# Optimization experiments

Measured on AMD Instinct MI355X. Metric: run time of the kernel, lower is better.

The kernel has to match this reference:

```python
import jax, jax.numpy as jnp
import numpy as np

HEADS = 16
DIM_HEAD = 64
QUERY_DIM = 1024
INNER = HEADS * DIM_HEAD
SCALE = DIM_HEAD ** -0.5


def setup_inputs() -> dict:
    key = jax.random.key(0)
    ks = jax.random.split(key, 6)
    B, N, M = 2, 2048, 2048
    x = jax.random.normal(ks[0], (B, N, QUERY_DIM), dtype=jnp.float32)
    context = jax.random.normal(ks[1], (B, M, QUERY_DIM), dtype=jnp.float32)
    s = QUERY_DIM ** -0.5
    # weights stored [in, out] so y = x @ W matches torch Linear(x) with W = weight.T
    Wq = jax.random.normal(ks[2], (QUERY_DIM, INNER), dtype=jnp.float32) * s
    Wk = jax.random.normal(ks[3], (QUERY_DIM, INNER), dtype=jnp.float32) * s
    Wv = jax.random.normal(ks[4], (QUERY_DIM, INNER), dtype=jnp.float32) * s
    Wo = jax.random.normal(ks[5], (INNER, QUERY_DIM), dtype=jnp.float32) * (INNER ** -0.5)
    return {"x": x, "context": context, "Wq": Wq, "Wk": Wk, "Wv": Wv, "Wo": Wo}


def reference(x, context, Wq, Wk, Wv, Wo):
    B, N, _ = x.shape
    M = context.shape[1]
    # projections -> [b, n, h, d]
    q = (x @ Wq).reshape(B, N, HEADS, DIM_HEAD)
    k = (context @ Wk).reshape(B, M, HEADS, DIM_HEAD)
    v = (context @ Wv).reshape(B, M, HEADS, DIM_HEAD)
    sim = jnp.einsum('bihd,bjhd->bhij', q, k) * SCALE  # [b, h, n, m]
    attn = jax.nn.softmax(sim, axis=-1)
    out = jnp.einsum('bhij,bjhd->bihd', attn, v)  # [b, n, h, d]
    out = out.reshape(B, N, INNER)
    return out @ Wo
```

## Files before the change

kernel.cpp:

```cpp
#include <hip/hip_runtime.h>
#include <hip/hip_bf16.h>


typedef __attribute__((ext_vector_type(8))) __bf16    bf16x8;
typedef __attribute__((ext_vector_type(4))) __bf16    bf16x4;
typedef __attribute__((ext_vector_type(4))) float     f32x4;

#define B_    2
#define H_    16
#define N_    2048
#define M_    2048
#define D_    64
#define QD_   1024

#define QSCALE 0.18033688011112042f

__device__ __forceinline__ void gld16(const __bf16* g, __bf16* l) {
    __builtin_amdgcn_global_load_lds(
        (const __attribute__((address_space(1))) unsigned int*)(g),
        (__attribute__((address_space(3))) unsigned int*)(l), 16, 0, 0);
}

__global__ __launch_bounds__(256) void prep(const float* __restrict__ x,
                                            const float* __restrict__ ctx,
                                            const float* __restrict__ w0,
                                            const float* __restrict__ w1,
                                            const float* __restrict__ w2,
                                            const float* __restrict__ w3,
                                            __bf16* __restrict__ xb,
                                            __bf16* __restrict__ cb,
                                            __bf16* __restrict__ t0,
                                            __bf16* __restrict__ t1,
                                            __bf16* __restrict__ t2,
                                            __bf16* __restrict__ t3) {
    __shared__ float tile[64][65];
    const int z = blockIdx.z;
    if (z < 2) {
        const float* src = z ? ctx : x;
        __bf16*      dst = z ? cb  : xb;
        const size_t base = (size_t)(blockIdx.y * 16 + blockIdx.x) * 16384;
#pragma unroll
        for (int p = 0; p < 16; ++p) {
            size_t i = base + p * 1024 + threadIdx.x * 4;
            float4 v = *reinterpret_cast<const float4*>(src + i);
            bf16x4 o;
            o.x = (__bf16)v.x; o.y = (__bf16)v.y; o.z = (__bf16)v.z; o.w = (__bf16)v.w;
            *reinterpret_cast<bf16x4*>(dst + i) = o;
        }
        return;
    }
    const int w = z - 2;
    const float* in = (w == 0) ? w0 : (w == 1) ? w1 : (w == 2) ? w2 : w3;
    __bf16*     out = (w == 0) ? t0 : (w == 1) ? t1 : (w == 2) ? t2 : t3;
    const int i0 = blockIdx.x * 64;
    const int o0 = blockIdx.y * 64;
    const int t  = threadIdx.x;
    const int r  = t >> 4;
    const int c4 = (t & 15) * 4;
#pragma unroll
    for (int p = 0; p < 4; ++p) {
        int row = p * 16 + r;
        float4 v = *reinterpret_cast<const float4*>(in + (size_t)(i0 + row) * QD_ + o0 + c4);
        tile[row][c4 + 0] = v.x; tile[row][c4 + 1] = v.y;
        tile[row][c4 + 2] = v.z; tile[row][c4 + 3] = v.w;
    }
    __syncthreads();
#pragma unroll
    for (int p = 0; p < 4; ++p) {
        int orow = p * 16 + r;
        bf16x4 o;
        o.x = (__bf16)tile[c4 + 0][orow];
        o.y = (__bf16)tile[c4 + 1][orow];
        o.z = (__bf16)tile[c4 + 2][orow];
        o.w = (__bf16)tile[c4 + 3][orow];
        *reinterpret_cast<bf16x4*>(out + (size_t)(o0 + orow) * QD_ + i0 + c4) = o;
    }
}

__global__ __launch_bounds__(256) void gemm_qkv(const __bf16* __restrict__ xb,
                                                const __bf16* __restrict__ cb,
                                                const __bf16* __restrict__ Wtq,
                                                const __bf16* __restrict__ Wtk,
                                                const __bf16* __restrict__ Wtv,
                                                __bf16* __restrict__ Qb,
                                                __bf16* __restrict__ Kb,
                                                __bf16* __restrict__ Vt) {
    __shared__ __align__(16) __bf16 POOL[16384];
    __bf16* const Al0 = POOL;
    __bf16* const Al1 = POOL + 4096;
    __bf16* const Bl0 = POOL + 8192;
    __bf16* const Bl1 = POOL + 12288;

    const int z = blockIdx.z;
    const __bf16* A_  = (z == 0) ? xb : cb;
    const __bf16* Bt_ = (z == 0) ? Wtq : (z == 1) ? Wtk : Wtv;

    const int tid  = threadIdx.x;
    const int wid  = tid >> 6;
    const int lane = tid & 63;
    const int l15  = lane & 15;
    const int lg   = lane >> 4;
    const int wr   = wid >> 1;
    const int wc   = wid & 1;
    const int rowBase = blockIdx.x * 128;
    const int colBase = blockIdx.y * 128;
    const int srow = wid * 32 + (lane >> 2);
    const int sg   = ((lane & 3) ^ ((srow >> 1) & 3)) * 8;
    const __bf16* Ag  = A_  + (size_t)(rowBase + srow) * QD_ + sg;
    const __bf16* Ag2 = Ag  + (size_t)16 * QD_;
    const __bf16* Bg  = Bt_ + (size_t)(colBase + srow) * QD_ + sg;
    const __bf16* Bg2 = Bg  + (size_t)16 * QD_;
    const int sOff  = (wid * 32) * 32;
    const int sOff2 = sOff + 16 * 32;
    int aoff[4], boff[4];
#pragma unroll
    for (int m = 0; m < 4; ++m) {
        int ra = wr * 64 + m * 16 + l15;
        int rb = wc * 64 + m * 16 + l15;
        aoff[m] = ra * 32 + ((lg ^ ((ra >> 1) & 3)) * 8);
        boff[m] = rb * 32 + ((lg ^ ((rb >> 1) & 3)) * 8);
    }
    f32x4 acc[4][4] = {};

#define GCOMPUTE(AL, BL)                                                                       \
    {                                                                                          \
        bf16x8 a[4], b[4];                                                                     \
        _Pragma("unroll")                                                                      \
        for (int m = 0; m < 4; ++m)                                                            \
            a[m] = *reinterpret_cast<const bf16x8*>(&(AL)[aoff[m]]);                           \
        _Pragma("unroll")                                                                      \
        for (int n = 0; n < 4; ++n)                                                            \
            b[n] = *reinterpret_cast<const bf16x8*>(&(BL)[boff[n]]);                           \
        _Pragma("unroll")                                                                      \
        for (int m = 0; m < 4; ++m)                                                            \
            _Pragma("unroll")                                                                  \
            for (int n = 0; n < 4; ++n)                                                        \
                acc[m][n] = __builtin_amdgcn_mfma_f32_16x16x32_bf16(a[m], b[n], acc[m][n], 0, 0, 0); \
    }

    gld16(Ag,  Al0 + sOff);
    gld16(Ag2, Al0 + sOff2);
    gld16(Bg,  Bl0 + sOff);
    gld16(Bg2, Bl0 + sOff2);
    __syncthreads();
    for (int t = 0; t < 32; t += 2) {
        if (t + 1 < 32) {
            int kn = (t + 1) * 32;
            gld16(Ag + kn,  Al1 + sOff);
            gld16(Ag2 + kn, Al1 + sOff2);
            gld16(Bg + kn,  Bl1 + sOff);
            gld16(Bg2 + kn, Bl1 + sOff2);
        }
        GCOMPUTE(Al0, Bl0)
        __syncthreads();
        if (t + 2 < 32) {
            int kn = (t + 2) * 32;
            gld16(Ag + kn,  Al0 + sOff);
            gld16(Ag2 + kn, Al0 + sOff2);
            gld16(Bg + kn,  Bl0 + sOff);
            gld16(Bg2 + kn, Bl0 + sOff2);
        }
        GCOMPUTE(Al1, Bl1)
        __syncthreads();
    }
#undef GCOMPUTE

#pragma unroll
    for (int m = 0; m < 4; ++m)
#pragma unroll
        for (int n = 0; n < 4; ++n)
#pragma unroll
            for (int r = 0; r < 4; ++r) {
                float v = acc[m][n][r];
                if (z == 0) v *= QSCALE;
                int rl = wr * 64 + m * 16 + lg * 4 + r;
                int cl = wc * 64 + n * 16 + l15;
                if (z == 2) POOL[cl * 128 + rl] = (__bf16)v;
                else        POOL[rl * 128 + cl] = (__bf16)v;
            }
    __syncthreads();

    const int prow0 = tid >> 4;
    const int pcol  = (tid & 15) * 8;
#pragma unroll
    for (int s = 0; s < 8; ++s) {
        int row = s * 16 + prow0;
        bf16x8 vv = *reinterpret_cast<const bf16x8*>(&POOL[row * 128 + pcol]);
        if (z == 2) {
            int cc = colBase + row, rr = rowBase + pcol;
            int b_ = rr >> 11, mm = rr & 2047, hh = cc >> 6, dd = cc & 63;
            *reinterpret_cast<bf16x8*>(&Vt[((size_t)(b_ * H_ + hh) * D_ + dd) * M_ + mm]) = vv;
        } else {
            int rr = rowBase + row, cc = colBase + pcol;
            int b_ = rr >> 11, nn = rr & 2047, hh = cc >> 6, dd = cc & 63;
            __bf16* dst = (z == 0) ? Qb : Kb;
            *reinterpret_cast<bf16x8*>(&dst[((size_t)(b_ * H_ + hh) * N_ + nn) * D_ + dd]) = vv;
        }
    }
}

__global__ __launch_bounds__(256) void gemm_out(const __bf16* __restrict__ AO,
                                                const __bf16* __restrict__ Wto,
                                                float* __restrict__ out) {
    __shared__ __align__(16) __bf16 POOL[16384];
    __bf16* const Al0 = POOL;
    __bf16* const Al1 = POOL + 4096;
    __bf16* const Bl0 = POOL + 8192;
    __bf16* const Bl1 = POOL + 10240;

    const int tid  = threadIdx.x;
    const int wid  = tid >> 6;
    const int lane = tid & 63;
    const int l15  = lane & 15;
    const int lg   = lane >> 4;
    const int wr   = wid >> 1;
    const int wc   = wid & 1;
    const int rowBase = blockIdx.x * 128;
    const int colBase = blockIdx.y * 64;
    const int srowA = wid * 32 + (lane >> 2);
    const int srowB = wid * 16 + (lane >> 2);
    const int sgA   = ((lane & 3) ^ ((srowA >> 1) & 3)) * 8;
    const int sgB   = ((lane & 3) ^ ((srowB >> 1) & 3)) * 8;
    const __bf16* Ag  = AO  + (size_t)(rowBase + srowA) * QD_ + sgA;
    const __bf16* Ag2 = Ag  + (size_t)16 * QD_;
    const __bf16* Bg  = Wto + (size_t)(colBase + srowB) * QD_ + sgB;
    const int sOffA  = (wid * 32) * 32;
    const int sOffA2 = sOffA + 16 * 32;
    const int sOffB  = (wid * 16) * 32;
    int aoff[4], boff[2];
#pragma unroll
    for (int m = 0; m < 4; ++m) {
        int ra = wr * 64 + m * 16 + l15;
        aoff[m] = ra * 32 + ((lg ^ ((ra >> 1) & 3)) * 8);
    }
#pragma unroll
    for (int n = 0; n < 2; ++n) {
        int rb = wc * 32 + n * 16 + l15;
        boff[n] = rb * 32 + ((lg ^ ((rb >> 1) & 3)) * 8);
    }
    f32x4 acc[4][2] = {};

#define GCOMPUTE2(AL, BL)                                                                      \
    {                                                                                          \
        bf16x8 a[4], b[2];                                                                     \
        _Pragma("unroll")                                                                      \
        for (int m = 0; m < 4; ++m)                                                            \
            a[m] = *reinterpret_cast<const bf16x8*>(&(AL)[aoff[m]]);                           \
        _Pragma("unroll")                                                                      \
        for (int n = 0; n < 2; ++n)                                                            \
            b[n] = *reinterpret_cast<const bf16x8*>(&(BL)[boff[n]]);                           \
        _Pragma("unroll")                                                                      \
        for (int m = 0; m < 4; ++m)                                                            \
            _Pragma("unroll")                                                                  \
            for (int n = 0; n < 2; ++n)                                                        \
                acc[m][n] = __builtin_amdgcn_mfma_f32_16x16x32_bf16(a[m], b[n], acc[m][n], 0, 0, 0); \
    }

    gld16(Ag,  Al0 + sOffA);
    gld16(Ag2, Al0 + sOffA2);
    gld16(Bg,  Bl0 + sOffB);
    __syncthreads();
    for (int t = 0; t < 32; t += 2) {
        if (t + 1 < 32) {
            int kn = (t + 1) * 32;
            gld16(Ag + kn,  Al1 + sOffA);
            gld16(Ag2 + kn, Al1 + sOffA2);
            gld16(Bg + kn,  Bl1 + sOffB);
        }
        GCOMPUTE2(Al0, Bl0)
        __syncthreads();
        if (t + 2 < 32) {
            int kn = (t + 2) * 32;
            gld16(Ag + kn,  Al0 + sOffA);
            gld16(Ag2 + kn, Al0 + sOffA2);
            gld16(Bg + kn,  Bl0 + sOffB);
        }
        GCOMPUTE2(Al1, Bl1)
        __syncthreads();
    }
#undef GCOMPUTE2

    float* FP = reinterpret_cast<float*>(POOL);
#pragma unroll
    for (int m = 0; m < 4; ++m)
#pragma unroll
        for (int n = 0; n < 2; ++n)
#pragma unroll
            for (int r = 0; r < 4; ++r) {
                int rl = wr * 64 + m * 16 + lg * 4 + r;
                int cl = wc * 32 + n * 16 + l15;
                FP[rl * 64 + cl] = acc[m][n][r];
            }
    __syncthreads();
    const int prow0 = tid >> 4;
    const int pcol4 = (tid & 15) * 4;
#pragma unroll
    for (int s = 0; s < 8; ++s) {
        int row = s * 16 + prow0;
        float4 vv = *reinterpret_cast<const float4*>(&FP[row * 64 + pcol4]);
        *reinterpret_cast<float4*>(&out[(size_t)(rowBase + row) * QD_ + colBase + pcol4]) = vv;
    }
}

__global__ __launch_bounds__(512, 4) void attn_kernel(const __bf16* __restrict__ Q,
                                                      const __bf16* __restrict__ K,
                                                      const __bf16* __restrict__ Vt,
                                                      __bf16* __restrict__ AO) {
    __shared__ __align__(16) __bf16 Klds[2][4096];
    __shared__ __align__(16) __bf16 Vlds[2][4096];

    const int logical = (blockIdx.x & 7) * 64 + (blockIdx.x >> 3);
    const int qt   = logical & 15;
    const int bh   = logical >> 4;
    const int b    = bh >> 4;
    const int h    = bh & 15;
    const int wid  = threadIdx.x >> 6;
    const int lane = threadIdx.x & 63;
    const int l15  = lane & 15;
    const int lg   = lane >> 4;
    const int qbase = qt * 128 + wid * 16;

    const __bf16* Qp = Q  + ((size_t)bh * N_ + qbase) * D_;
    const __bf16* Kp = K  + (size_t)bh * M_ * D_;
    const __bf16* Vp = Vt + (size_t)bh * D_ * M_;

    const int rg   = lane >> 3;
    const int ch   = lane & 7;
    const int skw  = (rg & 3) | ((wid & 1) << 2);
    const int kc   = (ch ^ skw) << 3;
    const int vc   = (ch ^ rg) << 3;
    const int srow = wid * 8 + rg;
    const int ldst = wid * 512;

#define STAGE(BUF, KV0)                                                        \
    gld16(Kp + (size_t)((KV0) + srow) * D_ + kc, &Klds[BUF][ldst]);            \
    gld16(Vp + (size_t)srow * M_ + (KV0) + vc,  &Vlds[BUF][ldst]);

    const int rm0 = ((l15 >> 2) * 8) + (l15 & 3);
    const int sq  = (l15 & 7) << 3;
    const int ak00 = rm0 * 64 + (( 0 + lg * 8) ^ sq);
    const int ak01 = rm0 * 64 + ((32 + lg * 8) ^ sq);
    const int ak10 = ak00 + 256;
    const int ak11 = ak01 + 256;
    const int av0 = l15 * 64 + (( 0 + lg * 8) ^ sq);
    const int av1 = l15 * 64 + ((32 + lg * 8) ^ sq);

    bf16x8 qf0 = *reinterpret_cast<const bf16x8*>(Qp + (size_t)l15 * D_ +      lg * 8);
    bf16x8 qf1 = *reinterpret_cast<const bf16x8*>(Qp + (size_t)l15 * D_ + 32 + lg * 8);

    bf16x8 onesf;
#pragma unroll
    for (int j = 0; j < 8; ++j) onesf[j] = (__bf16)1.0f;

    f32x4 o0 = {}, o1 = {}, o2 = {}, o3 = {}, ors = {};

#define COMPUTE(KB, VB, KOFF, AV)                                                               \
    {                                                                                           \
        bf16x8 k00 = *reinterpret_cast<const bf16x8*>((KB) + ak00 + (KOFF));                    \
        bf16x8 k01 = *reinterpret_cast<const bf16x8*>((KB) + ak01 + (KOFF));                    \
        bf16x8 k10 = *reinterpret_cast<const bf16x8*>((KB) + ak10 + (KOFF));                    \
        bf16x8 k11 = *reinterpret_cast<const bf16x8*>((KB) + ak11 + (KOFF));                    \
        bf16x8 v0  = *reinterpret_cast<const bf16x8*>((VB) + (AV));                             \
        bf16x8 v1  = *reinterpret_cast<const bf16x8*>((VB) + (AV) + 1024);                      \
        bf16x8 v2  = *reinterpret_cast<const bf16x8*>((VB) + (AV) + 2048);                      \
        bf16x8 v3  = *reinterpret_cast<const bf16x8*>((VB) + (AV) + 3072);                      \
        f32x4 s0 = {}, s1 = {};                                                                 \
        s0 = __builtin_amdgcn_mfma_f32_16x16x32_bf16(k00, qf0, s0, 0, 0, 0);                    \
        s0 = __builtin_amdgcn_mfma_f32_16x16x32_bf16(k01, qf1, s0, 0, 0, 0);                    \
        s1 = __builtin_amdgcn_mfma_f32_16x16x32_bf16(k10, qf0, s1, 0, 0, 0);                    \
        s1 = __builtin_amdgcn_mfma_f32_16x16x32_bf16(k11, qf1, s1, 0, 0, 0);                    \
        bf16x8 pf;                                                                              \
        pf[0] = (__bf16)__builtin_amdgcn_exp2f(s0[0]);                                          \
        pf[1] = (__bf16)__builtin_amdgcn_exp2f(s0[1]);                                          \
        pf[2] = (__bf16)__builtin_amdgcn_exp2f(s0[2]);                                          \
        pf[3] = (__bf16)__builtin_amdgcn_exp2f(s0[3]);                                          \
        pf[4] = (__bf16)__builtin_amdgcn_exp2f(s1[0]);                                          \
        pf[5] = (__bf16)__builtin_amdgcn_exp2f(s1[1]);                                          \
        pf[6] = (__bf16)__builtin_amdgcn_exp2f(s1[2]);                                          \
        pf[7] = (__bf16)__builtin_amdgcn_exp2f(s1[3]);                                          \
        ors = __builtin_amdgcn_mfma_f32_16x16x32_bf16(pf, onesf, ors, 0, 0, 0);                 \
        o0 = __builtin_amdgcn_mfma_f32_16x16x32_bf16(pf, v0, o0, 0, 0, 0);                      \
        o1 = __builtin_amdgcn_mfma_f32_16x16x32_bf16(pf, v1, o1, 0, 0, 0);                      \
        o2 = __builtin_amdgcn_mfma_f32_16x16x32_bf16(pf, v2, o2, 0, 0, 0);                      \
        o3 = __builtin_amdgcn_mfma_f32_16x16x32_bf16(pf, v3, o3, 0, 0, 0);                      \
    }

    STAGE(0, 0)
    __syncthreads();

    for (int t = 0; t < 32; t += 2) {
        if (t + 1 < 32) { STAGE(1, (t + 1) * 64) }
        COMPUTE(Klds[0], Vlds[0], 0,    av0)
        COMPUTE(Klds[0], Vlds[0], 2048, av1)
        __syncthreads();
        if (t + 2 < 32) { STAGE(0, (t + 2) * 64) }
        COMPUTE(Klds[1], Vlds[1], 0,    av0)
        COMPUTE(Klds[1], Vlds[1], 2048, av1)
        __syncthreads();
    }
#undef STAGE
#undef COMPUTE

#pragma unroll
    for (int r = 0; r < 4; ++r) {
        float inv = 1.0f / ors[r];
        size_t row = ((size_t)b * N_ + qbase + lg * 4 + r) * QD_ + h * D_ + l15;
        AO[row +  0] = (__bf16)(o0[r] * inv);
        AO[row + 16] = (__bf16)(o1[r] * inv);
        AO[row + 32] = (__bf16)(o2[r] * inv);
        AO[row + 48] = (__bf16)(o3[r] * inv);
    }
}

extern "C" void kernel_launch(void* const* d_in, const int* in_sizes, int n_in,
                              void* d_out, int out_size, void* d_ws, size_t ws_size,
                              hipStream_t stream) {
    const float* x   = (const float*)d_in[0];
    const float* ctx = (const float*)d_in[1];
    const float* Wq  = (const float*)d_in[2];
    const float* Wk  = (const float*)d_in[3];
    const float* Wv  = (const float*)d_in[4];
    const float* Wo  = (const float*)d_in[5];

    char* ws = (char*)d_ws;
    __bf16* xb  = (__bf16*)(ws);
    __bf16* cb  = (__bf16*)(ws + (8u  << 20));
    __bf16* Wtq = (__bf16*)(ws + (16u << 20));
    __bf16* Wtk = (__bf16*)(ws + (18u << 20));
    __bf16* Wtv = (__bf16*)(ws + (20u << 20));
    __bf16* Wto = (__bf16*)(ws + (22u << 20));
    __bf16* Qb  = (__bf16*)(ws + (24u << 20));
    __bf16* Kb  = (__bf16*)(ws + (32u << 20));
    __bf16* Vt  = (__bf16*)(ws + (40u << 20));
    __bf16* AO  = (__bf16*)(ws + (48u << 20));

    prep<<<dim3(16, 16, 6), 256, 0, stream>>>(x, ctx, Wq, Wk, Wv, Wo,
                                              xb, cb, Wtq, Wtk, Wtv, Wto);
    gemm_qkv<<<dim3(32, 8, 3), 256, 0, stream>>>(xb, cb, Wtq, Wtk, Wtv, Qb, Kb, Vt);
    attn_kernel<<<512, 512, 0, stream>>>(Qb, Kb, Vt, AO);
    gemm_out<<<dim3(32, 16), 256, 0, stream>>>(AO, Wto, (float*)d_out);
}
```

Baseline: 109.1 us.

## Process 32 query rows per wave in attention to reuse K/V fragments

The attention kernel now runs 4 waves of 256 threads per block instead of 8, and each wave handles 32 query rows instead of 16. Each K and V fragment read from LDS therefore feeds two sets of MFMAs, halving LDS reads per unit of compute. Each thread now issues four global-to-LDS loads per stage instead of two, so the same 64-row tile is still staged per block, and the swizzle indices are rewritten to match. The cost is roughly double the accumulator and score registers per wave and fewer waves per block, which may lower occupancy and latency hiding.

```diff
diff --git a/kernel.cpp b/kernel.cpp
--- a/kernel.cpp
+++ b/kernel.cpp
@@ -302,10 +302,10 @@
     }
 }
 
-__global__ __launch_bounds__(512, 4) void attn_kernel(const __bf16* __restrict__ Q,
-                                                      const __bf16* __restrict__ K,
-                                                      const __bf16* __restrict__ Vt,
-                                                      __bf16* __restrict__ AO) {
+__global__ __launch_bounds__(256) void attn_kernel(const __bf16* __restrict__ Q,
+                                                   const __bf16* __restrict__ K,
+                                                   const __bf16* __restrict__ Vt,
+                                                   __bf16* __restrict__ AO) {
     __shared__ __align__(16) __bf16 Klds[2][4096];
     __shared__ __align__(16) __bf16 Vlds[2][4096];
 
@@ -318,41 +318,53 @@
     const int lane = threadIdx.x & 63;
     const int l15  = lane & 15;
     const int lg   = lane >> 4;
-    const int qbase = qt * 128 + wid * 16;
+    const int qbase = qt * 128 + wid * 32;
 
     const __bf16* Qp = Q  + ((size_t)bh * N_ + qbase) * D_;
     const __bf16* Kp = K  + (size_t)bh * M_ * D_;
     const __bf16* Vp = Vt + (size_t)bh * D_ * M_;
 
-    const int rg   = lane >> 3;
-    const int ch   = lane & 7;
-    const int skw  = (rg & 3) | ((wid & 1) << 2);
-    const int kc   = (ch ^ skw) << 3;
-    const int vc   = (ch ^ rg) << 3;
-    const int srow = wid * 8 + rg;
-    const int ldst = wid * 512;
-
-#define STAGE(BUF, KV0)                                                        \
-    gld16(Kp + (size_t)((KV0) + srow) * D_ + kc, &Klds[BUF][ldst]);            \
-    gld16(Vp + (size_t)srow * M_ + (KV0) + vc,  &Vlds[BUF][ldst]);
+    const int srow = (wid << 4) + (lane >> 3);
+    const int scol = (lane & 7) << 3;
+    const int sk0  = (lane >> 3) & 3;
+    const int sk1  = sk0 | 4;
+    const int sv   = lane >> 3;
+    const int kc0  = scol ^ (sk0 << 3);
+    const int kc1  = scol ^ (sk1 << 3);
+    const int vc   = scol ^ (sv  << 3);
+    __bf16* kl0 = &Klds[0][wid * 1024];
+    __bf16* kl1 = &Klds[1][wid * 1024];
+    __bf16* vl0 = &Vlds[0][wid * 1024];
+    __bf16* vl1 = &Vlds[1][wid * 1024];
+
+#define STAGE(KL, VL, KV0)                                                     \
+    gld16(Kp + (size_t)((KV0) + srow)     * D_ + kc0, (KL));                   \
+    gld16(Kp + (size_t)((KV0) + srow + 8) * D_ + kc1, (KL) + 512);             \
+    gld16(Vp + (size_t)(srow)     * M_ + (KV0) + vc,  (VL));                   \
+    gld16(Vp + (size_t)(srow + 8) * M_ + (KV0) + vc,  (VL) + 512);
 
     const int rm0 = ((l15 >> 2) * 8) + (l15 & 3);
-    const int sq  = (l15 & 7) << 3;
-    const int ak00 = rm0 * 64 + (( 0 + lg * 8) ^ sq);
-    const int ak01 = rm0 * 64 + ((32 + lg * 8) ^ sq);
+    const int skq = (l15 & 3) | (((l15 >> 2) & 1) << 2);
+    const int svq = l15 & 7;
+    const int ak00 = rm0 * 64 + (( 0 + lg * 8) ^ (skq << 3));
+    const int ak01 = rm0 * 64 + ((32 + lg * 8) ^ (skq << 3));
     const int ak10 = ak00 + 256;
     const int ak11 = ak01 + 256;
-    const int av0 = l15 * 64 + (( 0 + lg * 8) ^ sq);
-    const int av1 = l15 * 64 + ((32 + lg * 8) ^ sq);
-
-    bf16x8 qf0 = *reinterpret_cast<const bf16x8*>(Qp + (size_t)l15 * D_ +      lg * 8);
-    bf16x8 qf1 = *reinterpret_cast<const bf16x8*>(Qp + (size_t)l15 * D_ + 32 + lg * 8);
+    const int av0 = l15 * 64 + (( 0 + lg * 8) ^ (svq << 3));
+    const int av1 = l15 * 64 + ((32 + lg * 8) ^ (svq << 3));
+
+    bf16x8 qf00 = *reinterpret_cast<const bf16x8*>(Qp + (size_t)(l15)      * D_ +      lg * 8);
+    bf16x8 qf01 = *reinterpret_cast<const bf16x8*>(Qp + (size_t)(l15)      * D_ + 32 + lg * 8);
+    bf16x8 qf10 = *reinterpret_cast<const bf16x8*>(Qp + (size_t)(16 + l15) * D_ +      lg * 8);
+    bf16x8 qf11 = *reinterpret_cast<const bf16x8*>(Qp + (size_t)(16 + l15) * D_ + 32 + lg * 8);
 
     bf16x8 onesf;
 #pragma unroll
     for (int j = 0; j < 8; ++j) onesf[j] = (__bf16)1.0f;
 
-    f32x4 o0 = {}, o1 = {}, o2 = {}, o3 = {}, ors = {};
+    f32x4 o00 = {}, o01 = {}, o10 = {}, o11 = {};
+    f32x4 o20 = {}, o21 = {}, o30 = {}, o31 = {};
+    f32x4 ors0 = {}, ors1 = {};
 
 #define COMPUTE(KB, VB, KOFF, AV)                                                               \
     {                                                                                           \
@@ -364,36 +376,53 @@
         bf16x8 v1  = *reinterpret_cast<const bf16x8*>((VB) + (AV) + 1024);                      \
         bf16x8 v2  = *reinterpret_cast<const bf16x8*>((VB) + (AV) + 2048);                      \
         bf16x8 v3  = *reinterpret_cast<const bf16x8*>((VB) + (AV) + 3072);                      \
-        f32x4 s0 = {}, s1 = {};                                                                 \
-        s0 = __builtin_amdgcn_mfma_f32_16x16x32_bf16(k00, qf0, s0, 0, 0, 0);                    \
-        s0 = __builtin_amdgcn_mfma_f32_16x16x32_bf16(k01, qf1, s0, 0, 0, 0);                    \
-        s1 = __builtin_amdgcn_mfma_f32_16x16x32_bf16(k10, qf0, s1, 0, 0, 0);                    \
-        s1 = __builtin_amdgcn_mfma_f32_16x16x32_bf16(k11, qf1, s1, 0, 0, 0);                    \
-        bf16x8 pf;                                                                              \
-        pf[0] = (__bf16)__builtin_amdgcn_exp2f(s0[0]);                                          \
-        pf[1] = (__bf16)__builtin_amdgcn_exp2f(s0[1]);                                          \
-        pf[2] = (__bf16)__builtin_amdgcn_exp2f(s0[2]);                                          \
-        pf[3] = (__bf16)__builtin_amdgcn_exp2f(s0[3]);                                          \
-        pf[4] = (__bf16)__builtin_amdgcn_exp2f(s1[0]);                                          \
-        pf[5] = (__bf16)__builtin_amdgcn_exp2f(s1[1]);                                          \
-        pf[6] = (__bf16)__builtin_amdgcn_exp2f(s1[2]);                                          \
-        pf[7] = (__bf16)__builtin_amdgcn_exp2f(s1[3]);                                          \
-        ors = __builtin_amdgcn_mfma_f32_16x16x32_bf16(pf, onesf, ors, 0, 0, 0);                 \
-        o0 = __builtin_amdgcn_mfma_f32_16x16x32_bf16(pf, v0, o0, 0, 0, 0);                      \
-        o1 = __builtin_amdgcn_mfma_f32_16x16x32_bf16(pf, v1, o1, 0, 0, 0);                      \
-        o2 = __builtin_amdgcn_mfma_f32_16x16x32_bf16(pf, v2, o2, 0, 0, 0);                      \
-        o3 = __builtin_amdgcn_mfma_f32_16x16x32_bf16(pf, v3, o3, 0, 0, 0);                      \
-    }
-
-    STAGE(0, 0)
+        f32x4 s00 = {}, s01 = {}, s10 = {}, s11 = {};                                           \
+        s00 = __builtin_amdgcn_mfma_f32_16x16x32_bf16(k00, qf00, s00, 0, 0, 0);                 \
+        s00 = __builtin_amdgcn_mfma_f32_16x16x32_bf16(k01, qf01, s00, 0, 0, 0);                 \
+        s01 = __builtin_amdgcn_mfma_f32_16x16x32_bf16(k00, qf10, s01, 0, 0, 0);                 \
+        s01 = __builtin_amdgcn_mfma_f32_16x16x32_bf16(k01, qf11, s01, 0, 0, 0);                 \
+        s10 = __builtin_amdgcn_mfma_f32_16x16x32_bf16(k10, qf00, s10, 0, 0, 0);                 \
+        s10 = __builtin_amdgcn_mfma_f32_16x16x32_bf16(k11, qf01, s10, 0, 0, 0);                 \
+        s11 = __builtin_amdgcn_mfma_f32_16x16x32_bf16(k10, qf10, s11, 0, 0, 0);                 \
+        s11 = __builtin_amdgcn_mfma_f32_16x16x32_bf16(k11, qf11, s11, 0, 0, 0);                 \
+        bf16x8 pf0, pf1;                                                                        \
+        pf0[0] = (__bf16)__builtin_amdgcn_exp2f(s00[0]);                                        \
+        pf0[1] = (__bf16)__builtin_amdgcn_exp2f(s00[1]);                                        \
+        pf0[2] = (__bf16)__builtin_amdgcn_exp2f(s00[2]);                                        \
+        pf0[3] = (__bf16)__builtin_amdgcn_exp2f(s00[3]);                                        \
+        pf0[4] = (__bf16)__builtin_amdgcn_exp2f(s10[0]);                                        \
+        pf0[5] = (__bf16)__builtin_amdgcn_exp2f(s10[1]);                                        \
+        pf0[6] = (__bf16)__builtin_amdgcn_exp2f(s10[2]);                                        \
+        pf0[7] = (__bf16)__builtin_amdgcn_exp2f(s10[3]);                                        \
+        pf1[0] = (__bf16)__builtin_amdgcn_exp2f(s01[0]);                                        \
+        pf1[1] = (__bf16)__builtin_amdgcn_exp2f(s01[1]);                                        \
+        pf1[2] = (__bf16)__builtin_amdgcn_exp2f(s01[2]);                                        \
+        pf1[3] = (__bf16)__builtin_amdgcn_exp2f(s01[3]);                                        \
+        pf1[4] = (__bf16)__builtin_amdgcn_exp2f(s11[0]);                                        \
+        pf1[5] = (__bf16)__builtin_amdgcn_exp2f(s11[1]);                                        \
+        pf1[6] = (__bf16)__builtin_amdgcn_exp2f(s11[2]);                                        \
+        pf1[7] = (__bf16)__builtin_amdgcn_exp2f(s11[3]);                                        \
+        ors0 = __builtin_amdgcn_mfma_f32_16x16x32_bf16(pf0, onesf, ors0, 0, 0, 0);              \
+        ors1 = __builtin_amdgcn_mfma_f32_16x16x32_bf16(pf1, onesf, ors1, 0, 0, 0);              \
+        o00 = __builtin_amdgcn_mfma_f32_16x16x32_bf16(pf0, v0, o00, 0, 0, 0);                   \
+        o01 = __builtin_amdgcn_mfma_f32_16x16x32_bf16(pf1, v0, o01, 0, 0, 0);                   \
+        o10 = __builtin_amdgcn_mfma_f32_16x16x32_bf16(pf0, v1, o10, 0, 0, 0);                   \
+        o11 = __builtin_amdgcn_mfma_f32_16x16x32_bf16(pf1, v1, o11, 0, 0, 0);                   \
+        o20 = __builtin_amdgcn_mfma_f32_16x16x32_bf16(pf0, v2, o20, 0, 0, 0);                   \
+        o21 = __builtin_amdgcn_mfma_f32_16x16x32_bf16(pf1, v2, o21, 0, 0, 0);                   \
+        o30 = __builtin_amdgcn_mfma_f32_16x16x32_bf16(pf0, v3, o30, 0, 0, 0);                   \
+        o31 = __builtin_amdgcn_mfma_f32_16x16x32_bf16(pf1, v3, o31, 0, 0, 0);                   \
+    }
+
+    STAGE(kl0, vl0, 0)
     __syncthreads();
 
     for (int t = 0; t < 32; t += 2) {
-        if (t + 1 < 32) { STAGE(1, (t + 1) * 64) }
+        if (t + 1 < 32) { STAGE(kl1, vl1, (t + 1) * 64) }
         COMPUTE(Klds[0], Vlds[0], 0,    av0)
         COMPUTE(Klds[0], Vlds[0], 2048, av1)
         __syncthreads();
-        if (t + 2 < 32) { STAGE(0, (t + 2) * 64) }
+        if (t + 2 < 32) { STAGE(kl0, vl0, (t + 2) * 64) }
         COMPUTE(Klds[1], Vlds[1], 0,    av0)
         COMPUTE(Klds[1], Vlds[1], 2048, av1)
         __syncthreads();
@@ -403,12 +432,18 @@
 
 #pragma unroll
     for (int r = 0; r < 4; ++r) {
-        float inv = 1.0f / ors[r];
-        size_t row = ((size_t)b * N_ + qbase + lg * 4 + r) * QD_ + h * D_ + l15;
-        AO[row +  0] = (__bf16)(o0[r] * inv);
-        AO[row + 16] = (__bf16)(o1[r] * inv);
-        AO[row + 32] = (__bf16)(o2[r] * inv);
-        AO[row + 48] = (__bf16)(o3[r] * inv);
+        float i0 = 1.0f / ors0[r];
+        float i1 = 1.0f / ors1[r];
+        size_t row0 = ((size_t)b * N_ + qbase + lg * 4 + r) * QD_ + h * D_ + l15;
+        size_t row1 = ((size_t)b * N_ + qbase + 16 + lg * 4 + r) * QD_ + h * D_ + l15;
+        AO[row0 +  0] = (__bf16)(o00[r] * i0);
+        AO[row0 + 16] = (__bf16)(o10[r] * i0);
+        AO[row0 + 32] = (__bf16)(o20[r] * i0);
+        AO[row0 + 48] = (__bf16)(o30[r] * i0);
+        AO[row1 +  0] = (__bf16)(o01[r] * i1);
+        AO[row1 + 16] = (__bf16)(o11[r] * i1);
+        AO[row1 + 32] = (__bf16)(o21[r] * i1);
+        AO[row1 + 48] = (__bf16)(o31[r] * i1);
     }
 }
 
@@ -437,6 +472,6 @@
     prep<<<dim3(16, 16, 6), 256, 0, stream>>>(x, ctx, Wq, Wk, Wv, Wo,
                                               xb, cb, Wtq, Wtk, Wtv, Wto);
     gemm_qkv<<<dim3(32, 8, 3), 256, 0, stream>>>(xb, cb, Wtq, Wtk, Wtv, Qb, Kb, Vt);
-    attn_kernel<<<512, 512, 0, stream>>>(Qb, Kb, Vt, AO);
+    attn_kernel<<<512, 256, 0, stream>>>(Qb, Kb, Vt, AO);
     gemm_out<<<dim3(32, 16), 256, 0, stream>>>(AO, Wto, (float*)d_out);
 }
```

Result: slower. 113.8 us (+4.3%).
